# Optimization experiments

Hardware: AMD Instinct MI355X
Metric: run time of the kernel (lower is better)

Reference implementation:

```python
import jax, jax.numpy as jnp
import numpy as np

N, P, D = 128, 256, 256
H, M = 16, 32            # num_heads, head_dim; output_dim = H*M = 512
OUT, HID = H * M, 2048


def setup_inputs() -> dict:
    key = jax.random.key(0)
    ks = jax.random.split(key, 7)
    s = 0.02
    return {
        "x": jax.random.normal(ks[0], (N, P, D), jnp.float32),
        "qkv_temporal": jax.random.normal(ks[1], (3, D, H, M), jnp.float32) * s,
        "qkv_point": jax.random.normal(ks[2], (3, H, M, H, M), jnp.float32) * s,
        "W1": jax.random.normal(ks[3], (OUT, HID), jnp.float32) * s,
        "b1": jnp.zeros((HID,), jnp.float32),
        "W2": jax.random.normal(ks[4], (HID, OUT), jnp.float32) * s,
        "b2": jnp.zeros((OUT,), jnp.float32),
    }


def reference(x, qkv_temporal, qkv_point, W1, b1, W2, b2):
    # ---- temporal attention (over frames i/I, per point j) ----
    qkv = jnp.einsum('wdhm,ijd->whmij', qkv_temporal, x)     # (3,H,M,N,P)
    q, k, v = qkv[0], qkv[1], qkv[2]
    scores = jnp.einsum('hmij,hmIj->hiIj', q, k)             # (H,N,N,P)
    weights = jax.nn.softmax(scores, axis=2)
    # NOTE: label order 'hIij' (positional) matches the original source exactly
    temporal = jnp.einsum('hIij,hmIj->hmij', weights, v)     # (H,M,N,P)
    # ---- point attention (over points j/J, per frame i) ----
    qkv = jnp.einsum('whmHM,HMij->whmij', qkv_point, temporal)  # (3,H,M,N,P)
    q, k, v = qkv[0], qkv[1], qkv[2]
    scores = jnp.einsum('hmij,hmiJ->hijJ', q, k)             # (H,N,P,P)
    weights = jax.nn.softmax(scores, axis=-1)
    pa = jnp.einsum('hijJ,hmiJ->ijhm', weights, v)           # (N,P,H,M)
    pa = pa.reshape(pa.shape[0], pa.shape[1], -1)            # (N,P,H*M)
    # ---- two-layer MLP (no activation, matching the source) ----
    h = pa @ W1 + b1
    return h @ W2 + b2
```

## Files before the change

### kernel.cpp

```cpp
#include <hip/hip_runtime.h>
#include <cstddef>
#include <cstdint>

constexpr int Nf = 128, Pp = 256, Dd = 256, Hh = 16, Mm = 32;
constexpr int OUTC = 512, HID = 2048, C3 = 1536;

typedef short short8 __attribute__((ext_vector_type(8)));
typedef float f32x4 __attribute__((ext_vector_type(4)));

__device__ inline unsigned short f2bf(float f) {
  unsigned u = __float_as_uint(f);
  u += 0x7fffu + ((u >> 16) & 1u);
  return (unsigned short)(u >> 16);
}
__device__ inline unsigned pk2(float a, float b) {
  unsigned r;
  asm("v_cvt_pk_bf16_f32 %0, %1, %2" : "=v"(r) : "v"(a), "v"(b));
  return r;
}

__global__ __launch_bounds__(256) void conv_x(const float* __restrict__ x,
                                              short* __restrict__ xb) {
  int idx = blockIdx.x * 256 + threadIdx.x;
  const float4* s = (const float4*)x + (size_t)idx * 2;
  float4 a = s[0], c = s[1];
  uint4 o;
  o.x = pk2(a.x, a.y); o.y = pk2(a.z, a.w);
  o.z = pk2(c.x, c.y); o.w = pk2(c.z, c.w);
  ((uint4*)xb)[idx] = o;
}

__global__ __launch_bounds__(256) void transpose_to_bf16(const float* __restrict__ in,
                                                         short* __restrict__ out,
                                                         int R, int C) {
  __shared__ float tile[64 * 65];
  const int t = threadIdx.x;
  const int rb = blockIdx.y * 64, cb = blockIdx.x * 64;
  const size_t sl = (size_t)blockIdx.z * R * C;
#pragma unroll
  for (int u = 0; u < 4; ++u) {
    int r = (t >> 4) + u * 16, c4 = (t & 15) * 4;
    float4 v = *(const float4*)(in + sl + (size_t)(rb + r) * C + cb + c4);
    tile[r * 65 + c4 + 0] = v.x;
    tile[r * 65 + c4 + 1] = v.y;
    tile[r * 65 + c4 + 2] = v.z;
    tile[r * 65 + c4 + 3] = v.w;
  }
  __syncthreads();
#pragma unroll
  for (int u = 0; u < 2; ++u) {
    int id = t + u * 256;
    int n = id >> 3, kg = id & 7;
    float a[8];
#pragma unroll
    for (int q = 0; q < 8; ++q) a[q] = tile[(kg * 8 + q) * 65 + n];
    uint4 o;
    o.x = pk2(a[0], a[1]); o.y = pk2(a[2], a[3]);
    o.z = pk2(a[4], a[5]); o.w = pk2(a[6], a[7]);
    *(uint4*)(out + sl + (size_t)(cb + n) * R + rb + kg * 8) = o;
  }
}

__global__ void repack_b2t(const float* __restrict__ Wp, short* __restrict__ B2t) {
  int idx = blockIdx.x * 256 + threadIdx.x;
  int c = idx >> 9, k = idx & 511;
  int w = c >> 9, h = (c >> 5) & 15, m = c & 31;
  int HH = k >> 5, MM = k & 31;
  B2t[idx] = (short)f2bf(Wp[(((w * Hh + h) * Mm + m) * Hh + HH) * Mm + MM]);
}

__global__ __launch_bounds__(256) void wc_splitk(const short* __restrict__ A,
                                                 const short* __restrict__ Bt,
                                                 float* __restrict__ part) {
  __shared__ short As[128 * 32];
  __shared__ short Bs[128 * 32];
  const int t = threadIdx.x;
  const int wv = t >> 6, ln = t & 63;
  const int wr = wv >> 1, wc = wv & 1;
  const int lr = ln & 15, kq = ln >> 4;
  const int row0 = blockIdx.y * 128, col0 = blockIdx.x * 128;
  const int k0 = blockIdx.z * 256;

  f32x4 acc[4][4];
#pragma unroll
  for (int i = 0; i < 4; ++i)
#pragma unroll
    for (int j = 0; j < 4; ++j) acc[i][j] = {0.f, 0.f, 0.f, 0.f};

  for (int kt = k0; kt < k0 + 256; kt += 32) {
#pragma unroll
    for (int u = 0; u < 2; ++u) {
      int seg = wv * 128 + u * 64 + ln;
      int r = seg >> 2, kg = seg & 3;
      const short* gp = A + (size_t)(row0 + r) * HID + kt + kg * 8;
      __builtin_amdgcn_global_load_lds(
          (const __attribute__((address_space(1))) void*)gp,
          (__attribute__((address_space(3))) void*)&As[(wv * 128 + u * 64) * 8], 16, 0, 0);
    }
#pragma unroll
    for (int u = 0; u < 2; ++u) {
      int seg = wv * 128 + u * 64 + ln;
      int r = seg >> 2, kg = seg & 3;
      const short* gp = Bt + (size_t)(col0 + r) * HID + kt + kg * 8;
      __builtin_amdgcn_global_load_lds(
          (const __attribute__((address_space(1))) void*)gp,
          (__attribute__((address_space(3))) void*)&Bs[(wv * 128 + u * 64) * 8], 16, 0, 0);
    }
    __syncthreads();
    short8 a[4], b[4];
#pragma unroll
    for (int ti = 0; ti < 4; ++ti)
      a[ti] = *(const short8*)&As[(wr * 64 + ti * 16 + lr) * 32 + kq * 8];
#pragma unroll
    for (int tj = 0; tj < 4; ++tj)
      b[tj] = *(const short8*)&Bs[(wc * 64 + tj * 16 + lr) * 32 + kq * 8];
#pragma unroll
    for (int ti = 0; ti < 4; ++ti)
#pragma unroll
      for (int tj = 0; tj < 4; ++tj)
        acc[ti][tj] = __builtin_amdgcn_mfma_f32_16x16x32_bf16(a[ti], b[tj], acc[ti][tj], 0, 0, 0);
    __syncthreads();
  }

#pragma unroll
  for (int tj = 0; tj < 4; ++tj) {
    int gcol = col0 + wc * 64 + tj * 16 + lr;
#pragma unroll
    for (int ti = 0; ti < 4; ++ti)
#pragma unroll
      for (int rg = 0; rg < 4; ++rg) {
        int grow = row0 + wr * 64 + ti * 16 + kq * 4 + rg;
        part[((size_t)blockIdx.z * 512 + grow) * 512 + gcol] = acc[ti][tj][rg];
      }
  }
}

__global__ __launch_bounds__(256) void wc_reduce(const float* __restrict__ part,
                                                 short* __restrict__ Wct) {
  int idx = blockIdx.x * 256 + threadIdx.x;
  float s = 0.f;
#pragma unroll
  for (int z = 0; z < 8; ++z) s += part[(size_t)z * 262144 + idx];
  Wct[idx] = (short)f2bf(s);
}

__global__ __launch_bounds__(256) void bc_partial(const float* __restrict__ b1,
                                                  const float* __restrict__ W2,
                                                  float* __restrict__ part) {
  const int z = blockIdx.x;
  const int t = threadIdx.x;
  float s0 = 0.f, s1 = 0.f;
#pragma unroll
  for (int hh = 0; hh < 32; ++hh) {
    int h = z * 32 + hh;
    float bv = b1[h];
    s0 += bv * W2[(size_t)h * OUTC + t];
    s1 += bv * W2[(size_t)h * OUTC + t + 256];
  }
  part[z * OUTC + t] = s0;
  part[z * OUTC + t + 256] = s1;
}

__global__ __launch_bounds__(256) void bc_finish(const float* __restrict__ part,
                                                 const float* __restrict__ b2,
                                                 float* __restrict__ bc) {
  int o = blockIdx.x * 256 + threadIdx.x;
  float s = b2[o];
#pragma unroll
  for (int z = 0; z < 64; ++z) s += part[z * OUTC + o];
  bc[o] = s;
}

template <int KDIM, int NCOLS, int AMAP, int EPI, int OUTT>
__global__ __launch_bounds__(256) void gemm_mfma(const short* __restrict__ A,
                                                 const short* __restrict__ Bt,
                                                 void* __restrict__ Cv,
                                                 const float* __restrict__ bias,
                                                 int j0, int pshift, int pc) {
  __shared__ __align__(16) short SH[16384];
  const int t = threadIdx.x;
  const int wv = t >> 6, ln = t & 63;
  const int wr = wv >> 1, wc = wv & 1;
  const int lr = ln & 15, kq = ln >> 4;

  constexpr int NBX = NCOLS / 128;
  constexpr int NT = KDIM / 32;
  int lin = blockIdx.y * NBX + blockIdx.x;
  int nblk = gridDim.x * gridDim.y;
  int bx, by;
  if ((nblk & 7) == 0) {
    int per = nblk >> 3;
    int id = (lin & 7) * per + (lin >> 3);
    bx = id % NBX; by = id / NBX;
  } else {
    bx = blockIdx.x; by = blockIdx.y;
  }
  const int row0 = by * 128, col0 = bx * 128;

  const int seg0 = wv * 128 + ln;
  const int seg1 = wv * 128 + 64 + ln;
  const int r0 = seg0 >> 2, r1 = seg1 >> 2;
  const int kg0 = (seg0 & 3) ^ ((r0 >> 1) & 3);
  const int kg1 = (seg1 & 3) ^ ((r1 >> 1) & 3);
  size_t arow0, arow1;
  {
    int rr = row0 + r0;
    if (AMAP == 0)      arow0 = (size_t)rr;
    else if (AMAP == 3) arow0 = (size_t)(((rr & 127) << 8) + (rr >> 7));
    else { int i = rr >> pshift, jj = rr & (pc - 1); arow0 = (size_t)((i << 8) + j0 + jj); }
    rr = row0 + r1;
    if (AMAP == 0)      arow1 = (size_t)rr;
    else if (AMAP == 3) arow1 = (size_t)(((rr & 127) << 8) + (rr >> 7));
    else { int i = rr >> pshift, jj = rr & (pc - 1); arow1 = (size_t)((i << 8) + j0 + jj); }
  }
  const size_t brow0 = (size_t)(col0 + r0), brow1 = (size_t)(col0 + r1);

  auto stage = [&](int buf, int tk) {
    const int kt = tk * 32;
    __builtin_amdgcn_global_load_lds(
        (const __attribute__((address_space(1))) void*)(A + arow0 * KDIM + kt + kg0 * 8),
        (__attribute__((address_space(3))) void*)&SH[buf * 4096 + (wv * 128) * 8], 16, 0, 0);
    __builtin_amdgcn_global_load_lds(
        (const __attribute__((address_space(1))) void*)(A + arow1 * KDIM + kt + kg1 * 8),
        (__attribute__((address_space(3))) void*)&SH[buf * 4096 + (wv * 128 + 64) * 8], 16, 0, 0);
    __builtin_amdgcn_global_load_lds(
        (const __attribute__((address_space(1))) void*)(Bt + brow0 * KDIM + kt + kg0 * 8),
        (__attribute__((address_space(3))) void*)&SH[8192 + buf * 4096 + (wv * 128) * 8], 16, 0, 0);
    __builtin_amdgcn_global_load_lds(
        (const __attribute__((address_space(1))) void*)(Bt + brow1 * KDIM + kt + kg1 * 8),
        (__attribute__((address_space(3))) void*)&SH[8192 + buf * 4096 + (wv * 128 + 64) * 8], 16, 0, 0);
  };

  f32x4 acc[4][4];
#pragma unroll
  for (int i = 0; i < 4; ++i)
#pragma unroll
    for (int j = 0; j < 4; ++j) acc[i][j] = {0.f, 0.f, 0.f, 0.f};

  const int slot = kq ^ ((lr >> 1) & 3);

  stage(0, 0);
  stage(1, 1);
  asm volatile("s_waitcnt vmcnt(4)" ::: "memory");
  __builtin_amdgcn_s_barrier();

  for (int tk = 0; tk < NT; ++tk) {
    const int cur = tk & 1;
    short8 a[4], b[4];
#pragma unroll
    for (int ti = 0; ti < 4; ++ti)
      a[ti] = *(const short8*)&SH[cur * 4096 + (wr * 64 + ti * 16 + lr) * 32 + slot * 8];
#pragma unroll
    for (int tj = 0; tj < 4; ++tj)
      b[tj] = *(const short8*)&SH[8192 + cur * 4096 + (wc * 64 + tj * 16 + lr) * 32 + slot * 8];
    __builtin_amdgcn_sched_barrier(0);
    asm volatile("s_waitcnt lgkmcnt(0)" ::: "memory");
    __builtin_amdgcn_sched_barrier(0);
    if (tk + 1 < NT) {
      __builtin_amdgcn_s_barrier();
      if (tk + 2 < NT) stage(cur, tk + 2);
    }
#pragma unroll
    for (int ti = 0; ti < 4; ++ti)
#pragma unroll
      for (int tj = 0; tj < 4; ++tj)
        acc[ti][tj] = __builtin_amdgcn_mfma_f32_16x16x32_bf16(a[ti], b[tj], acc[ti][tj], 0, 0, 0);
    if (tk + 1 < NT) {
      if (tk + 2 < NT) {
        asm volatile("s_waitcnt vmcnt(4)" ::: "memory");
      } else {
        asm volatile("s_waitcnt vmcnt(0)" ::: "memory");
      }
      __builtin_amdgcn_s_barrier();
      __builtin_amdgcn_sched_barrier(0);
    }
  }

  if (EPI == 0 || EPI == 1) {
#pragma unroll
    for (int tj = 0; tj < 4; ++tj) {
      int gcol = col0 + wc * 64 + tj * 16 + lr;
      float bv = (EPI == 0) ? bias[gcol] : 0.f;
#pragma unroll
      for (int ti = 0; ti < 4; ++ti) {
#pragma unroll
        for (int rg = 0; rg < 4; ++rg) {
          int grow = row0 + wr * 64 + ti * 16 + kq * 4 + rg;
          float val = acc[ti][tj][rg];
          if (EPI == 0) {
            val += bv;
            if (OUTT == 0) ((short*)Cv)[(size_t)grow * NCOLS + gcol] = (short)f2bf(val);
            else           ((float*)Cv)[(size_t)grow * NCOLS + gcol] = val;
          } else {
            int w = gcol >> 9, h = (gcol >> 5) & 15, m = gcol & 31;
            int i = grow >> pshift, jj = grow & (pc - 1);
            size_t addr = (((size_t)(w * Hh + h) * pc + jj) * Nf + i) * Mm + m;
            ((short*)Cv)[addr] = (short)f2bf(val);
          }
        }
      }
    }
  } else {
    __builtin_amdgcn_s_barrier();
#pragma unroll
    for (int ti = 0; ti < 4; ++ti)
#pragma unroll
      for (int tj = 0; tj < 4; ++tj) {
        int c = wc * 64 + tj * 16 + lr;
        int q = c >> 5, m = c & 31;
#pragma unroll
        for (int rg = 0; rg < 4; ++rg) {
          int g = wr * 64 + ti * 16 + kq * 4 + rg;
          SH[q * 4096 + g * 32 + (m ^ ((g & 4) << 2))] = (short)f2bf(acc[ti][tj][rg]);
        }
      }
    __syncthreads();
#pragma unroll
    for (int u = 0; u < 8; ++u) {
      int id = u * 256 + t;
      int q = id >> 9, rem = id & 511, g = rem >> 2, mc = (rem & 3) * 8;
      uint4 v = *(const uint4*)&SH[q * 4096 + g * 32 + (mc ^ ((g & 4) << 2))];
      int gc = col0 + q * 32;
      int w = gc >> 9, h = (gc >> 5) & 15;
      size_t base;
      if (EPI == 3) base = ((size_t)(w * Hh + h) * 256 + (row0 >> 7)) * 4096;
      else          base = (((size_t)(w * Hh + h) * pc + (row0 >> 8)) * 256 + (row0 & 255)) * 32;
      *(uint4*)((short*)Cv + base + g * 32 + mc) = v;
    }
  }
}

__global__ __launch_bounds__(256, 4) void temporal_attn_mfma(const short* __restrict__ T,
                                                             short* __restrict__ At,
                                                             int j0, int jcShift) {
  constexpr int KsO = 0, VtO = 4096, WtO = 8448, RsO = 17664;
  __shared__ __align__(16) short lds[18176];
  float* rs = (float*)&lds[RsO];
  const int JC = 1 << jcShift;
  const int h  = blockIdx.x >> jcShift;
  const int jj = blockIdx.x & (JC - 1);
  const int t  = threadIdx.x;
  const int wv = t >> 6, ln = t & 63;
  const int wr = wv >> 1, wc = wv & 1;
  const int lr = ln & 15, kq = ln >> 4;
  const size_t WC = (size_t)(Hh << jcShift) * 4096;
  const short* qb = T + (size_t)(h * JC + jj) * 4096;
  const short* kb = qb + WC;
  const short* vb = qb + 2 * WC;

  const int lnoff = (ln >> 2) * 32 + (((ln & 3) ^ ((ln >> 3) & 3)) * 8);
  const int qkslot = (kq ^ ((lr >> 1) & 3)) * 8;

  short8 af[4];
#pragma unroll
  for (int ti = 0; ti < 4; ++ti)
    af[ti] = *(const short8*)(qb + (wr * 64 + ti * 16 + lr) * 32 + kq * 8);

#pragma unroll
  for (int u = 0; u < 2; ++u) {
    int seg = wv * 2 + u;
    __builtin_amdgcn_global_load_lds(
        (const __attribute__((address_space(1))) void*)(kb + seg * 512 + lnoff),
        (__attribute__((address_space(3))) void*)&lds[KsO + seg * 512], 16, 0, 0);
  }
#pragma unroll
  for (int u = 0; u < 2; ++u) {
    int idx = t + u * 256;
    int I = idx >> 2, g = idx & 3;
    uint4 v = *(const uint4*)(vb + idx * 8);
    unsigned w0 = v.x, w1 = v.y, w2 = v.z, w3 = v.w;
    if (g & 1) { unsigned tp = w0; w0 = w1; w1 = w2; w2 = w3; w3 = tp; }
    if (g & 2) { unsigned t0 = w0, t1 = w1; w0 = w2; w1 = w3; w2 = t0; w3 = t1; }
    const unsigned wa[4] = {w0, w1, w2, w3};
    int m0 = g * 8, g2 = g * 2;
#pragma unroll
    for (int k = 0; k < 4; ++k) {
      int q = (2 * k + g2) & 7;
      lds[VtO + (m0 + q) * 136 + I]     = (short)(wa[k] & 0xffffu);
      lds[VtO + (m0 + q + 1) * 136 + I] = (short)(wa[k] >> 16);
    }
  }
  __syncthreads();

  short8 bf[4];
#pragma unroll
  for (int tj = 0; tj < 4; ++tj)
    bf[tj] = *(const short8*)&lds[KsO + (wc * 64 + tj * 16 + lr) * 32 + qkslot];
  f32x4 e[4][4];
#pragma unroll
  for (int ti = 0; ti < 4; ++ti)
#pragma unroll
    for (int tj = 0; tj < 4; ++tj) e[ti][tj] = {0.f, 0.f, 0.f, 0.f};
#pragma unroll
  for (int ti = 0; ti < 4; ++ti)
#pragma unroll
    for (int tj = 0; tj < 4; ++tj)
      e[ti][tj] = __builtin_amdgcn_mfma_f32_16x16x32_bf16(af[ti], bf[tj], e[ti][tj], 0, 0, 0);

  float part[4][4];
#pragma unroll
  for (int ti = 0; ti < 4; ++ti)
#pragma unroll
    for (int r = 0; r < 4; ++r) {
      float p = 0.f;
#pragma unroll
      for (int tj = 0; tj < 4; ++tj) {
        float ex = __expf(e[ti][tj][r]);
        e[ti][tj][r] = ex;
        p += ex;
      }
      part[ti][r] = p;
    }
#pragma unroll
  for (int msk = 1; msk <= 8; msk <<= 1)
#pragma unroll
    for (int ti = 0; ti < 4; ++ti)
#pragma unroll
      for (int r = 0; r < 4; ++r)
        part[ti][r] += __shfl_xor(part[ti][r], msk, 64);
  if (lr == 0) {
#pragma unroll
    for (int ti = 0; ti < 4; ++ti)
#pragma unroll
      for (int r = 0; r < 4; ++r)
        rs[wc * 128 + wr * 64 + ti * 16 + kq * 4 + r] = part[ti][r];
  }
  __syncthreads();

#pragma unroll
  for (int ti = 0; ti < 4; ++ti)
#pragma unroll
    for (int r = 0; r < 4; ++r) {
      int I = wr * 64 + ti * 16 + kq * 4 + r;
      float inv = 1.f / (rs[I] + rs[128 + I]);
#pragma unroll
      for (int tj = 0; tj < 4; ++tj) e[ti][tj][r] *= inv;
    }

  f32x4 o[2][2];
#pragma unroll
  for (int tr = 0; tr < 2; ++tr)
#pragma unroll
    for (int tm = 0; tm < 2; ++tm) o[tr][tm] = {0.f, 0.f, 0.f, 0.f};
#pragma unroll
  for (int p = 0; p < 2; ++p) {
    if (p) __syncthreads();
    if (wr == p) {
#pragma unroll
      for (int ti = 0; ti < 4; ++ti)
#pragma unroll
        for (int tj = 0; tj < 4; ++tj) {
          int i = wc * 64 + tj * 16 + lr;
          int Ib = ti * 16 + kq * 4;
          uint2 pk;
          pk.x = pk2(e[ti][tj][0], e[ti][tj][1]);
          pk.y = pk2(e[ti][tj][2], e[ti][tj][3]);
          *(uint2*)&lds[WtO + i * 72 + Ib] = pk;
        }
    }
    __syncthreads();
#pragma unroll
    for (int ks = 0; ks < 2; ++ks) {
      short8 ea[2], vf[2];
#pragma unroll
      for (int tr = 0; tr < 2; ++tr)
        ea[tr] = *(const short8*)&lds[WtO + (wv * 32 + tr * 16 + lr) * 72 + ks * 32 + kq * 8];
#pragma unroll
      for (int tm = 0; tm < 2; ++tm)
        vf[tm] = *(const short8*)&lds[VtO + (tm * 16 + lr) * 136 + p * 64 + ks * 32 + kq * 8];
#pragma unroll
      for (int tr = 0; tr < 2; ++tr)
#pragma unroll
        for (int tm = 0; tm < 2; ++tm)
          o[tr][tm] = __builtin_amdgcn_mfma_f32_16x16x32_bf16(ea[tr], vf[tm], o[tr][tm], 0, 0, 0);
    }
  }
#pragma unroll
  for (int tr = 0; tr < 2; ++tr)
#pragma unroll
    for (int tm = 0; tm < 2; ++tm)
#pragma unroll
      for (int r = 0; r < 4; ++r) {
        int row = wv * 32 + tr * 16 + kq * 4 + r;
        lds[row * 40 + tm * 16 + lr] = (short)f2bf(o[tr][tm][r]);
      }
  __syncthreads();
#pragma unroll
  for (int u = 0; u < 2; ++u) {
    int idx = t + u * 256;
    int i = idx >> 2, mg = idx & 3;
    uint4 vv = *(const uint4*)&lds[i * 40 + mg * 8];
    *(uint4*)(At + ((size_t)(i * Pp + j0 + jj) * OUTC + h * 32 + mg * 8)) = vv;
  }
}

__global__ __launch_bounds__(256, 4) void point_attn_mfma(const short* __restrict__ P,
                                                          short* __restrict__ PA,
                                                          int icShift) {
  constexpr int KsO = 0, VtO = 4096, EO = 8448, CsO = 17664;
  __shared__ __align__(16) short lds[18432];
  float* cs    = (float*)&lds[CsO];
  float* denom = cs + 256;
  const int IC = 1 << icShift;
  const int bx = blockIdx.x;
  const int h    = bx >> (icShift + 1);
  const int rem  = bx & ((IC << 1) - 1);
  const int ii   = rem >> 1;
  const int half = rem & 1;
  const int t  = threadIdx.x;
  const int wv = t >> 6, ln = t & 63;
  const int wr = wv >> 1, wc = wv & 1;
  const int lr = ln & 15, kq = ln >> 4;
  const size_t WC = (size_t)(Hh << icShift) * 8192;
  const short* qb = P + (size_t)(h * IC + ii) * 8192 + half * 4096;
  const short* kb = P + WC + (size_t)(h * IC + ii) * 8192;
  const short* vb = kb + WC;

  const int lnoff = (ln >> 2) * 32 + (((ln & 3) ^ ((ln >> 3) & 3)) * 8);
  const int qkslot = (kq ^ ((lr >> 1) & 3)) * 8;

  short8 bf[4];
#pragma unroll
  for (int tj = 0; tj < 4; ++tj)
    bf[tj] = *(const short8*)(qb + (wc * 64 + tj * 16 + lr) * 32 + kq * 8);

  f32x4 o[2][2];
#pragma unroll
  for (int tr = 0; tr < 2; ++tr)
#pragma unroll
    for (int tm = 0; tm < 2; ++tm) o[tr][tm] = {0.f, 0.f, 0.f, 0.f};

  for (int chunk = 0; chunk < 2; ++chunk) {
    const int Jb = chunk * 128;
    if (chunk) __syncthreads();
#pragma unroll
    for (int u = 0; u < 2; ++u) {
      int seg = wv * 2 + u;
      __builtin_amdgcn_global_load_lds(
          (const __attribute__((address_space(1))) void*)(kb + Jb * 32 + seg * 512 + lnoff),
          (__attribute__((address_space(3))) void*)&lds[KsO + seg * 512], 16, 0, 0);
    }
    if (chunk == 0) {
      if (t < 128) denom[t] = 0.f;
    }
#pragma unroll
    for (int u = 0; u < 2; ++u) {
      int idx = t + u * 256;
      int Jl = idx >> 2, g = idx & 3;
      uint4 v = *(const uint4*)(vb + Jb * 32 + idx * 8);
      unsigned w0 = v.x, w1 = v.y, w2 = v.z, w3 = v.w;
      if (g & 1) { unsigned tp = w0; w0 = w1; w1 = w2; w2 = w3; w3 = tp; }
      if (g & 2) { unsigned t0 = w0, t1 = w1; w0 = w2; w1 = w3; w2 = t0; w3 = t1; }
      const unsigned wa[4] = {w0, w1, w2, w3};
      int m0 = g * 8, g2 = g * 2;
#pragma unroll
      for (int k = 0; k < 4; ++k) {
        int q = (2 * k + g2) & 7;
        lds[VtO + (m0 + q) * 136 + Jl]     = (short)(wa[k] & 0xffffu);
        lds[VtO + (m0 + q + 1) * 136 + Jl] = (short)(wa[k] >> 16);
      }
    }
    __syncthreads();

    short8 af[4];
#pragma unroll
    for (int ti = 0; ti < 4; ++ti)
      af[ti] = *(const short8*)&lds[KsO + (wr * 64 + ti * 16 + lr) * 32 + qkslot];
    f32x4 e[4][4];
#pragma unroll
    for (int ti = 0; ti < 4; ++ti)
#pragma unroll
      for (int tj = 0; tj < 4; ++tj) e[ti][tj] = {0.f, 0.f, 0.f, 0.f};
#pragma unroll
    for (int ti = 0; ti < 4; ++ti)
#pragma unroll
      for (int tj = 0; tj < 4; ++tj)
        e[ti][tj] = __builtin_amdgcn_mfma_f32_16x16x32_bf16(af[ti], bf[tj], e[ti][tj], 0, 0, 0);

    float cp[4] = {0.f, 0.f, 0.f, 0.f};
#pragma unroll
    for (int ti = 0; ti < 4; ++ti)
#pragma unroll
      for (int tj = 0; tj < 4; ++tj)
#pragma unroll
        for (int r = 0; r < 4; ++r) {
          float ex = __expf(e[ti][tj][r]);
          e[ti][tj][r] = ex;
          cp[tj] += ex;
        }
#pragma unroll
    for (int tj = 0; tj < 4; ++tj) {
      cp[tj] += __shfl_xor(cp[tj], 16, 64);
      cp[tj] += __shfl_xor(cp[tj], 32, 64);
    }
    if (kq == 0) {
#pragma unroll
      for (int tj = 0; tj < 4; ++tj)
        cs[wr * 128 + wc * 64 + tj * 16 + lr] = cp[tj];
    }

#pragma unroll
    for (int p = 0; p < 2; ++p) {
      if (p) __syncthreads();
      if (wr == p) {
#pragma unroll
        for (int ti = 0; ti < 4; ++ti)
#pragma unroll
          for (int tj = 0; tj < 4; ++tj) {
            int j  = wc * 64 + tj * 16 + lr;
            int Jl = ti * 16 + kq * 4;
            uint2 pk;
            pk.x = pk2(e[ti][tj][0], e[ti][tj][1]);
            pk.y = pk2(e[ti][tj][2], e[ti][tj][3]);
            *(uint2*)&lds[EO + j * 72 + Jl] = pk;
          }
      }
      __syncthreads();
      if (p == 0 && t < 128) denom[t] += cs[t] + cs[128 + t];
#pragma unroll
      for (int ks = 0; ks < 2; ++ks) {
        short8 ea[2], vf[2];
#pragma unroll
        for (int tr = 0; tr < 2; ++tr)
          ea[tr] = *(const short8*)&lds[EO + (wv * 32 + tr * 16 + lr) * 72 + ks * 32 + kq * 8];
#pragma unroll
        for (int tm = 0; tm < 2; ++tm)
          vf[tm] = *(const short8*)&lds[VtO + (tm * 16 + lr) * 136 + p * 64 + ks * 32 + kq * 8];
#pragma unroll
        for (int tr = 0; tr < 2; ++tr)
#pragma unroll
          for (int tm = 0; tm < 2; ++tm)
            o[tr][tm] = __builtin_amdgcn_mfma_f32_16x16x32_bf16(ea[tr], vf[tm], o[tr][tm], 0, 0, 0);
      }
    }
  }
  __syncthreads();

#pragma unroll
  for (int tr = 0; tr < 2; ++tr)
#pragma unroll
    for (int r = 0; r < 4; ++r) {
      int row = wv * 32 + tr * 16 + kq * 4 + r;
      float rinv = 1.f / denom[row];
#pragma unroll
      for (int tm = 0; tm < 2; ++tm)
        lds[row * 40 + tm * 16 + lr] = (short)f2bf(o[tr][tm][r] * rinv);
    }
  __syncthreads();
#pragma unroll
  for (int u = 0; u < 2; ++u) {
    int idx = t + u * 256;
    int jl = idx >> 2, mg = idx & 3;
    uint4 vv = *(const uint4*)&lds[jl * 40 + mg * 8];
    *(uint4*)(PA + ((size_t)(ii * Pp + half * 128 + jl) * OUTC + h * 32 + mg * 8)) = vv;
  }
}

extern "C" void kernel_launch(void* const* d_in, const int* in_sizes, int n_in,
                              void* d_out, int out_size, void* d_ws, size_t ws_size,
                              hipStream_t stream) {
  const float* x  = (const float*)d_in[0];
  const float* Wt = (const float*)d_in[1];
  const float* Wp = (const float*)d_in[2];
  const float* W1 = (const float*)d_in[3];
  const float* b1 = (const float*)d_in[4];
  const float* W2 = (const float*)d_in[5];
  const float* b2 = (const float*)d_in[6];
  float* out = (float*)d_out;
  short* ws  = (short*)d_ws;

  const size_t fixedH = 8388608 + 16777216 + 393216 + 786432 + 1048576 + 1048576
                      + 262144 + 1024 + 4194304 + 65536;
  size_t availH = ws_size / 2;
  size_t chF; int JC, IC;
  if      (availH >= fixedH + 50331648) { chF = 50331648; JC = 256; IC = 128; }
  else if (availH >= fixedH + 12582912) { chF = 12582912; JC = 64;  IC = 32;  }
  else if (availH >= fixedH + 6291456)  { chF = 6291456;  JC = 32;  IC = 16;  }
  else                                  { chF = 3145728;  JC = 16;  IC = 8;   }
  short* CH  = ws;
  short* xbf = CH + chF;
  short* At  = xbf + 8388608;
  short* B1t = At + 16777216;
  short* B2t = B1t + 393216;
  short* W1b = B2t + 786432;
  short* W2t = W1b + 1048576;
  short* Wct = W2t + 1048576;
  float* bcF   = (float*)(Wct + 262144);
  float* partF = (float*)(Wct + 262144 + 1024);
  float* bcP   = (float*)(Wct + 262144 + 1024 + 4194304);
  const int jcS = __builtin_ctz((unsigned)JC);
  const int icS = __builtin_ctz((unsigned)IC);

  conv_x<<<4096, 256, 0, stream>>>(x, xbf);
  conv_x<<<512, 256, 0, stream>>>(W1, W1b);
  transpose_to_bf16<<<dim3(8, 4, 3), 256, 0, stream>>>(Wt, B1t, 256, 512);
  repack_b2t<<<3072, 256, 0, stream>>>(Wp, B2t);
  transpose_to_bf16<<<dim3(8, 32, 1), 256, 0, stream>>>(W2, W2t, 2048, 512);

  wc_splitk<<<dim3(4, 4, 8), 256, 0, stream>>>(W2t, W1b, partF);
  wc_reduce<<<1024, 256, 0, stream>>>(partF, Wct);
  bc_partial<<<64, 256, 0, stream>>>(b1, W2, bcP);
  bc_finish<<<2, 256, 0, stream>>>(bcP, b2, bcF);

  if (JC == 256) {
    gemm_mfma<256, 1536, 3, 3, 0><<<dim3(12, 256), 256, 0, stream>>>(xbf, B1t, CH, nullptr, 0, 0, 256);
    temporal_attn_mfma<<<Hh * 256, 256, 0, stream>>>(CH, At, 0, 8);
    gemm_mfma<512, 1536, 0, 2, 0><<<dim3(12, 256), 256, 0, stream>>>(At, B2t, CH, nullptr, 0, 0, 128);
    point_attn_mfma<<<Hh * 128 * 2, 256, 0, stream>>>(CH, At, 7);
  } else {
    for (int j0 = 0; j0 < Pp; j0 += JC) {
      gemm_mfma<256, 1536, 1, 1, 0><<<dim3(12, JC), 256, 0, stream>>>(xbf, B1t, CH, nullptr, j0, jcS, JC);
      temporal_attn_mfma<<<Hh * JC, 256, 0, stream>>>(CH, At, j0, jcS);
    }
    for (int i0 = 0; i0 < Nf; i0 += IC) {
      short* Arows = At + (size_t)i0 * Pp * OUTC;
      gemm_mfma<512, 1536, 0, 2, 0><<<dim3(12, IC * 2), 256, 0, stream>>>(Arows, B2t, CH, nullptr, 0, 0, IC);
      point_attn_mfma<<<Hh * IC * 2, 256, 0, stream>>>(CH, Arows, icS);
    }
  }

  gemm_mfma<512, 512, 0, 0, 1><<<dim3(4, 256), 256, 0, stream>>>(At, Wct, out, bcF, 0, 0, 0);
}
```

Before: 370.4 us.

## Store attention outputs head-major and read them with new GEMM A-maps

```diff
diff --git a/kernel.cpp b/kernel.cpp
--- a/kernel.cpp
+++ b/kernel.cpp
@@ -202,26 +202,31 @@
   const int r0 = seg0 >> 2, r1 = seg1 >> 2;
   const int kg0 = (seg0 & 3) ^ ((r0 >> 1) & 3);
   const int kg1 = (seg1 & 3) ^ ((r1 >> 1) & 3);
-  size_t arow0, arow1;
+  size_t aoff0, aoff1;
   {
     int rr = row0 + r0;
-    if (AMAP == 0)      arow0 = (size_t)rr;
-    else if (AMAP == 3) arow0 = (size_t)(((rr & 127) << 8) + (rr >> 7));
-    else { int i = rr >> pshift, jj = rr & (pc - 1); arow0 = (size_t)((i << 8) + j0 + jj); }
+    if (AMAP == 0)      aoff0 = (size_t)rr * KDIM;
+    else if (AMAP == 3) aoff0 = (size_t)(((rr & 127) << 8) + (rr >> 7)) * KDIM;
+    else if (AMAP == 4) aoff0 = (size_t)rr * 32;
+    else if (AMAP == 5) aoff0 = (size_t)(((rr & 255) << 7) + (rr >> 8)) * 32;
+    else { int i = rr >> pshift, jj = rr & (pc - 1); aoff0 = (size_t)((i << 8) + j0 + jj) * KDIM; }
     rr = row0 + r1;
-    if (AMAP == 0)      arow1 = (size_t)rr;
-    else if (AMAP == 3) arow1 = (size_t)(((rr & 127) << 8) + (rr >> 7));
-    else { int i = rr >> pshift, jj = rr & (pc - 1); arow1 = (size_t)((i << 8) + j0 + jj); }
+    if (AMAP == 0)      aoff1 = (size_t)rr * KDIM;
+    else if (AMAP == 3) aoff1 = (size_t)(((rr & 127) << 8) + (rr >> 7)) * KDIM;
+    else if (AMAP == 4) aoff1 = (size_t)rr * 32;
+    else if (AMAP == 5) aoff1 = (size_t)(((rr & 255) << 7) + (rr >> 8)) * 32;
+    else { int i = rr >> pshift, jj = rr & (pc - 1); aoff1 = (size_t)((i << 8) + j0 + jj) * KDIM; }
   }
   const size_t brow0 = (size_t)(col0 + r0), brow1 = (size_t)(col0 + r1);
 
   auto stage = [&](int buf, int tk) {
     const int kt = tk * 32;
+    const size_t kb = (AMAP >= 4) ? (size_t)tk * 1048576 : (size_t)kt;
     __builtin_amdgcn_global_load_lds(
-        (const __attribute__((address_space(1))) void*)(A + arow0 * KDIM + kt + kg0 * 8),
+        (const __attribute__((address_space(1))) void*)(A + aoff0 + kb + kg0 * 8),
         (__attribute__((address_space(3))) void*)&SH[buf * 4096 + (wv * 128) * 8], 16, 0, 0);
     __builtin_amdgcn_global_load_lds(
-        (const __attribute__((address_space(1))) void*)(A + arow1 * KDIM + kt + kg1 * 8),
+        (const __attribute__((address_space(1))) void*)(A + aoff1 + kb + kg1 * 8),
         (__attribute__((address_space(3))) void*)&SH[buf * 4096 + (wv * 128 + 64) * 8], 16, 0, 0);
     __builtin_amdgcn_global_load_lds(
         (const __attribute__((address_space(1))) void*)(Bt + brow0 * KDIM + kt + kg0 * 8),
@@ -330,6 +335,7 @@
   }
 }
 
+template <int LAYOUT>
 __global__ __launch_bounds__(256, 4) void temporal_attn_mfma(const short* __restrict__ T,
                                                              short* __restrict__ At,
                                                              int j0, int jcShift) {
@@ -485,15 +491,27 @@
         lds[row * 40 + tm * 16 + lr] = (short)f2bf(o[tr][tm][r]);
       }
   __syncthreads();
-#pragma unroll
-  for (int u = 0; u < 2; ++u) {
-    int idx = t + u * 256;
-    int i = idx >> 2, mg = idx & 3;
-    uint4 vv = *(const uint4*)&lds[i * 40 + mg * 8];
-    *(uint4*)(At + ((size_t)(i * Pp + j0 + jj) * OUTC + h * 32 + mg * 8)) = vv;
-  }
-}
-
+  if (LAYOUT == 1) {
+    const size_t base = (size_t)(h * 256 + j0 + jj) * 4096;
+#pragma unroll
+    for (int u = 0; u < 2; ++u) {
+      int idx = t + u * 256;
+      int i = idx >> 2, mg = idx & 3;
+      uint4 vv = *(const uint4*)&lds[i * 40 + mg * 8];
+      *(uint4*)(At + base + i * 32 + mg * 8) = vv;
+    }
+  } else {
+#pragma unroll
+    for (int u = 0; u < 2; ++u) {
+      int idx = t + u * 256;
+      int i = idx >> 2, mg = idx & 3;
+      uint4 vv = *(const uint4*)&lds[i * 40 + mg * 8];
+      *(uint4*)(At + ((size_t)(i * Pp + j0 + jj) * OUTC + h * 32 + mg * 8)) = vv;
+    }
+  }
+}
+
+template <int LAYOUT>
 __global__ __launch_bounds__(256, 4) void point_attn_mfma(const short* __restrict__ P,
                                                           short* __restrict__ PA,
                                                           int icShift) {
@@ -647,12 +665,23 @@
         lds[row * 40 + tm * 16 + lr] = (short)f2bf(o[tr][tm][r] * rinv);
     }
   __syncthreads();
-#pragma unroll
-  for (int u = 0; u < 2; ++u) {
-    int idx = t + u * 256;
-    int jl = idx >> 2, mg = idx & 3;
-    uint4 vv = *(const uint4*)&lds[jl * 40 + mg * 8];
-    *(uint4*)(PA + ((size_t)(ii * Pp + half * 128 + jl) * OUTC + h * 32 + mg * 8)) = vv;
+  if (LAYOUT == 1) {
+    const size_t base = ((size_t)(h * 128 + ii) * 256 + half * 128) * 32;
+#pragma unroll
+    for (int u = 0; u < 2; ++u) {
+      int idx = t + u * 256;
+      int jl = idx >> 2, mg = idx & 3;
+      uint4 vv = *(const uint4*)&lds[jl * 40 + mg * 8];
+      *(uint4*)(PA + base + jl * 32 + mg * 8) = vv;
+    }
+  } else {
+#pragma unroll
+    for (int u = 0; u < 2; ++u) {
+      int idx = t + u * 256;
+      int jl = idx >> 2, mg = idx & 3;
+      uint4 vv = *(const uint4*)&lds[jl * 40 + mg * 8];
+      *(uint4*)(PA + ((size_t)(ii * Pp + half * 128 + jl) * OUTC + h * 32 + mg * 8)) = vv;
+    }
   }
 }
 
@@ -704,20 +733,20 @@
 
   if (JC == 256) {
     gemm_mfma<256, 1536, 3, 3, 0><<<dim3(12, 256), 256, 0, stream>>>(xbf, B1t, CH, nullptr, 0, 0, 256);
-    temporal_attn_mfma<<<Hh * 256, 256, 0, stream>>>(CH, At, 0, 8);
-    gemm_mfma<512, 1536, 0, 2, 0><<<dim3(12, 256), 256, 0, stream>>>(At, B2t, CH, nullptr, 0, 0, 128);
-    point_attn_mfma<<<Hh * 128 * 2, 256, 0, stream>>>(CH, At, 7);
+    temporal_attn_mfma<1><<<Hh * 256, 256, 0, stream>>>(CH, At, 0, 8);
+    gemm_mfma<512, 1536, 5, 2, 0><<<dim3(12, 256), 256, 0, stream>>>(At, B2t, CH, nullptr, 0, 0, 128);
+    point_attn_mfma<1><<<Hh * 128 * 2, 256, 0, stream>>>(CH, At, 7);
+    gemm_mfma<512, 512, 4, 0, 1><<<dim3(4, 256), 256, 0, stream>>>(At, Wct, out, bcF, 0, 0, 0);
   } else {
     for (int j0 = 0; j0 < Pp; j0 += JC) {
       gemm_mfma<256, 1536, 1, 1, 0><<<dim3(12, JC), 256, 0, stream>>>(xbf, B1t, CH, nullptr, j0, jcS, JC);
-      temporal_attn_mfma<<<Hh * JC, 256, 0, stream>>>(CH, At, j0, jcS);
+      temporal_attn_mfma<0><<<Hh * JC, 256, 0, stream>>>(CH, At, j0, jcS);
     }
     for (int i0 = 0; i0 < Nf; i0 += IC) {
       short* Arows = At + (size_t)i0 * Pp * OUTC;
       gemm_mfma<512, 1536, 0, 2, 0><<<dim3(12, IC * 2), 256, 0, stream>>>(Arows, B2t, CH, nullptr, 0, 0, IC);
-      point_attn_mfma<<<Hh * IC * 2, 256, 0, stream>>>(CH, Arows, icS);
-    }
-  }
-
-  gemm_mfma<512, 512, 0, 0, 1><<<dim3(4, 256), 256, 0, stream>>>(At, Wct, out, bcF, 0, 0, 0);
-}
+      point_attn_mfma<0><<<Hh * IC * 2, 256, 0, stream>>>(CH, Arows, icS);
+    }
+    gemm_mfma<512, 512, 0, 0, 1><<<dim3(4, 256), 256, 0, stream>>>(At, Wct, out, bcF, 0, 0, 0);
+  }
+}
```

New measurement: 370.2 us. About the same (-0.0%).
